# Kernel tuning notes

Measured on AMD Instinct MI355X. Metric: run time of the kernel, lower is better.

Reference implementation:

```python
import jax, jax.numpy as jnp
import numpy as np

B, L, D = 4, 2048, 512
H, DK, DV = 8, 64, 64


def setup_inputs() -> dict:
    key = jax.random.key(0)
    ks = jax.random.split(key, 12)
    s = 0.02
    return {
        "query": jax.random.normal(ks[0], (B, L, D), jnp.float32),
        "key": jax.random.normal(ks[1], (B, L, D), jnp.float32),
        "value": jax.random.normal(ks[2], (B, L, D), jnp.float32),
        "attention_mask": jax.random.normal(ks[3], (1, 1, L, L), jnp.float32),
        "Wq": jax.random.normal(ks[4], (D, H * DK), jnp.float32) * s,
        "bq": jnp.zeros((H * DK,), jnp.float32),
        "Wk": jax.random.normal(ks[5], (D, H * DK), jnp.float32) * s,
        "bk": jnp.zeros((H * DK,), jnp.float32),
        "Wv": jax.random.normal(ks[6], (D, H * DV), jnp.float32) * s,
        "bv": jnp.zeros((H * DV,), jnp.float32),
        "Wo": jax.random.normal(ks[7], (H * DV, D), jnp.float32) * s,
        "bo": jnp.zeros((D,), jnp.float32),
    }


def reference(query, key, value, attention_mask, Wq, bq, Wk, bk, Wv, bv, Wo, bo):
    sz_b, len_q, _ = query.shape
    len_k = key.shape[1]
    # projections -> [B, L, H, d]
    q = (query @ Wq + bq).reshape(sz_b, len_q, H, DK)
    k = (key @ Wk + bk).reshape(sz_b, len_k, H, DK)
    v = (value @ Wv + bv).reshape(sz_b, len_k, H, DV)
    # permute(2,0,1,3): heads first -> [H, B, L, d]
    q = jnp.transpose(q, (2, 0, 1, 3))
    k = jnp.transpose(k, (2, 0, 1, 3))
    v = jnp.transpose(v, (2, 0, 1, 3))
    scale = 1.0 / jnp.sqrt(jnp.asarray(DK, q.dtype))
    scores = jnp.einsum('hbqd,hbkd->hbqk', q, k) * scale + attention_mask
    attn = jax.nn.softmax(scores, axis=-1)
    x = jnp.einsum('hbqk,hbkd->hbqd', attn, v)  # [H, B, Lq, Dv]
    # faithful to torch: transpose(1,2) -> [H, Lq, B, Dv] then view(B, Lq, H*Dv)
    x = jnp.transpose(x, (0, 2, 1, 3)).reshape(sz_b, len_q, H * DV)
    return x @ Wo + bo
```

## Files before the change

kernel.cpp:

```cpp
#include <hip/hip_runtime.h>

#define SEQ    2048
#define DMODEL 512
#define NHEAD  8
#define HDIM   64
#define BATCH  4

#define LOG2E  1.4426950408889634f
#define QSCALE 0.18033688011112042f

typedef float f32x4  __attribute__((ext_vector_type(4)));
typedef float f32x16 __attribute__((ext_vector_type(16)));
typedef _Float16 h16x8 __attribute__((ext_vector_type(8)));
typedef _Float16 h16x2 __attribute__((ext_vector_type(2)));

union U4H { uint4 u; h16x8 h; };
union U1H2 { unsigned int u; h16x2 h; };

static __device__ inline h16x2 pkrtz(float a, float b) {
    return __builtin_bit_cast(h16x2, __builtin_amdgcn_cvt_pkrtz(a, b));
}
static __device__ inline unsigned short f2h(float x) {
    _Float16 h = (_Float16)x;
    return __builtin_bit_cast(unsigned short, h);
}
static __device__ inline void async_cp16(const void* g, void* l) {
    __builtin_amdgcn_global_load_lds(
        (const __attribute__((address_space(1))) unsigned int*)g,
        (__attribute__((address_space(3))) unsigned int*)l,
        16, 0, 0);
}

__global__ __launch_bounds__(256) void transpose_cast_w(
    const float* __restrict__ s0, const float* __restrict__ s1,
    const float* __restrict__ s2, const float* __restrict__ s3,
    unsigned short* __restrict__ d0, unsigned short* __restrict__ d1,
    unsigned short* __restrict__ d2, unsigned short* __restrict__ d3)
{
    const float* S; unsigned short* D;
    switch (blockIdx.z) {
        case 0: S = s0; D = d0; break;
        case 1: S = s1; D = d1; break;
        case 2: S = s2; D = d2; break;
        default: S = s3; D = d3; break;
    }
    __shared__ float T[32][33];
    const int t = threadIdx.x;
    const int r = t >> 3, c = (t & 7) * 4;
    const int k0 = blockIdx.x * 32, n0 = blockIdx.y * 32;
    float4 v = *(const float4*)&S[(size_t)(k0 + r) * DMODEL + n0 + c];
    T[r][c] = v.x; T[r][c + 1] = v.y; T[r][c + 2] = v.z; T[r][c + 3] = v.w;
    __syncthreads();
    ushort4 o;
    o.x = f2h(T[c + 0][r]); o.y = f2h(T[c + 1][r]);
    o.z = f2h(T[c + 2][r]); o.w = f2h(T[c + 3][r]);
    *(ushort4*)&D[(size_t)(n0 + r) * DMODEL + k0 + c] = o;
}

__global__ __launch_bounds__(256) void prep_mask(
    const float* __restrict__ mask, unsigned short* __restrict__ mp)
{
    int i = blockIdx.x * 256 + threadIdx.x;
    int k = (i * 4) & (SEQ - 1);
    int q = (i * 4) >> 11;
    float4 v = ((const float4*)mask)[i];
    int kt = k >> 6, kl = k & 63;
    int mt = kl >> 5, g = (kl >> 3) & 3, hl = (kl >> 2) & 1;
    size_t base = ((size_t)kt * SEQ + q) * 64 + hl * 32 + mt * 16 + g * 4;
    ushort4 o;
    o.x = f2h(__builtin_amdgcn_exp2f(v.x * LOG2E));
    o.y = f2h(__builtin_amdgcn_exp2f(v.y * LOG2E));
    o.z = f2h(__builtin_amdgcn_exp2f(v.z * LOG2E));
    o.w = f2h(__builtin_amdgcn_exp2f(v.w * LOG2E));
    *(ushort4*)&mp[base] = o;
}

__global__ __launch_bounds__(256) void transpose_v(
    const unsigned short* __restrict__ vb, unsigned short* __restrict__ vT)
{
    const int t = threadIdx.x;
    const int key0 = blockIdx.x * 64;
    const int bh = blockIdx.y, b = bh >> 3, h = bh & 7;
    #pragma unroll
    for (int p = 0; p < 2; p++) {
        int cid = p * 256 + t;
        int dv = cid >> 3, kch = cid & 7;
        unsigned short tmp[8];
        #pragma unroll
        for (int j = 0; j < 8; j++)
            tmp[j] = vb[(size_t)(b * SEQ + key0 + kch * 8 + j) * DMODEL + h * HDIM + dv];
        uint4 o;
        o.x = tmp[0] | ((unsigned)tmp[1] << 16);
        o.y = tmp[2] | ((unsigned)tmp[3] << 16);
        o.z = tmp[4] | ((unsigned)tmp[5] << 16);
        o.w = tmp[6] | ((unsigned)tmp[7] << 16);
        *(uint4*)&vT[(size_t)((b * NHEAD + h) * HDIM + dv) * SEQ + key0 + kch * 8] = o;
    }
}

template <int A_FP32, int OUT_F16>
static __device__ inline void gemm_core(
    const void* __restrict__ Ap, const unsigned short* __restrict__ Bt,
    const float* __restrict__ bias, void* __restrict__ Cout, float oscale,
    int bm, int bn)
{
    __shared__ __align__(16) unsigned short As[128 * 32];
    __shared__ __align__(16) unsigned short Bs[128 * 32];

    const int t = threadIdx.x;
    const int lane = t & 63, w = t >> 6;
    const int wm = w >> 1, wn = w & 1;
    const int c = lane & 15, quad = lane >> 4;

    f32x4 acc[4][4] = {};

    for (int k0 = 0; k0 < DMODEL; k0 += 32) {
        if (A_FP32) {
            const float* Af = (const float*)Ap;
            #pragma unroll
            for (int p = 0; p < 4; p++) {
                int cid = p * 256 + t;
                int row = cid >> 3, fc = cid & 7;
                float4 av = *(const float4*)&Af[(size_t)(bm + row) * DMODEL + k0 + fc * 4];
                U1H2 lo, hi;
                lo.h = pkrtz(av.x, av.y);
                hi.h = pkrtz(av.z, av.w);
                uint2 st = make_uint2(lo.u, hi.u);
                *(uint2*)&As[row * 32 + fc * 4] = st;
            }
        } else {
            const unsigned short* Ab = (const unsigned short*)Ap;
            #pragma unroll
            for (int i = 0; i < 2; i++) {
                int row = 32 * w + 16 * i + (lane >> 2);
                const unsigned short* gp = Ab + (size_t)(bm + row) * DMODEL + k0 + (lane & 3) * 8;
                async_cp16(gp, &As[(32 * w + 16 * i) * 32]);
            }
        }
        #pragma unroll
        for (int i = 0; i < 2; i++) {
            int row = 32 * w + 16 * i + (lane >> 2);
            const unsigned short* gp = Bt + (size_t)(bn + row) * DMODEL + k0 + (lane & 3) * 8;
            async_cp16(gp, &Bs[(32 * w + 16 * i) * 32]);
        }
        __syncthreads();

        U4H af[4], bf[4];
        #pragma unroll
        for (int mt = 0; mt < 4; mt++)
            af[mt].u = *(const uint4*)&As[(wm * 64 + mt * 16 + c) * 32 + quad * 8];
        #pragma unroll
        for (int nt = 0; nt < 4; nt++)
            bf[nt].u = *(const uint4*)&Bs[(wn * 64 + nt * 16 + c) * 32 + quad * 8];
        #pragma unroll
        for (int mt = 0; mt < 4; mt++)
            #pragma unroll
            for (int nt = 0; nt < 4; nt++)
                acc[mt][nt] = __builtin_amdgcn_mfma_f32_16x16x32_f16(
                    af[mt].h, bf[nt].h, acc[mt][nt], 0, 0, 0);
        __syncthreads();
    }

    #pragma unroll
    for (int nt = 0; nt < 4; nt++) {
        int ng = bn + wn * 64 + nt * 16 + c;
        float bv = bias[ng];
        #pragma unroll
        for (int mt = 0; mt < 4; mt++) {
            #pragma unroll
            for (int r = 0; r < 4; r++) {
                int mg = bm + wm * 64 + mt * 16 + quad * 4 + r;
                float v = (acc[mt][nt][r] + bv) * oscale;
                if (OUT_F16)
                    ((unsigned short*)Cout)[(size_t)mg * DMODEL + ng] = f2h(v);
                else
                    ((float*)Cout)[(size_t)mg * DMODEL + ng] = v;
            }
        }
    }
}

struct QKVArgs {
    const float *A0, *A1, *A2;
    const unsigned short *W0, *W1, *W2;
    const float *b0, *b1, *b2;
    unsigned short *o0, *o1, *o2;
};

__global__ __launch_bounds__(256) void gemm_qkv(QKVArgs a) {
    const float* A; const unsigned short* W; const float* bias;
    unsigned short* out; float sc;
    switch (blockIdx.z) {
        case 0: A = a.A0; W = a.W0; bias = a.b0; out = a.o0; sc = QSCALE; break;
        case 1: A = a.A1; W = a.W1; bias = a.b1; out = a.o1; sc = 1.0f;  break;
        default: A = a.A2; W = a.W2; bias = a.b2; out = a.o2; sc = 1.0f; break;
    }
    gemm_core<1, 1>(A, W, bias, out, sc, blockIdx.y * 128, blockIdx.x * 128);
}

__global__ __launch_bounds__(256) void gemm_fin(
    const unsigned short* __restrict__ A, const unsigned short* __restrict__ W,
    const float* __restrict__ bias, float* __restrict__ C) {
    gemm_core<0, 0>(A, W, bias, C, 1.0f, blockIdx.y * 128, blockIdx.x * 128);
}

__global__ __launch_bounds__(256, 2) void attn4(
    const unsigned short* __restrict__ qb, const unsigned short* __restrict__ kb,
    const unsigned short* __restrict__ vT, const unsigned short* __restrict__ emp,
    unsigned short* __restrict__ X)
{
    __shared__ __align__(16) unsigned short Ks[8 * 65 * 8];
    __shared__ __align__(16) unsigned short Vs[8 * 65 * 8];

    const int t = threadIdx.x;
    const int lane = t & 63, w = t >> 6;
    const int c32 = lane & 31, hl = lane >> 5;
    const int bh = blockIdx.x, b = bh >> 3, head = bh & 7;
    const int q0 = blockIdx.y * 128;
    const int qg = q0 + w * 32 + c32;

    const unsigned short* qrow = qb + ((size_t)b * SEQ + qg) * DMODEL + head * HDIM;
    U4H Qf[4];
    #pragma unroll
    for (int s = 0; s < 4; s++)
        Qf[s].u = *(const uint4*)&qrow[s * 16 + hl * 8];

    const unsigned short* kgb = kb + (size_t)b * SEQ * DMODEL + head * HDIM;
    const unsigned short* vgb = vT + (size_t)bh * HDIM * SEQ;

    const int r8p = t >> 3;
    const int chp = t & 7;

    uint4 kreg[2], vreg[2];
    #pragma unroll
    for (int p = 0; p < 2; p++) {
        int r8 = p * 32 + r8p;
        kreg[p] = *(const uint4*)&kgb[(size_t)r8 * DMODEL + chp * 8];
        vreg[p] = *(const uint4*)&vgb[(size_t)r8 * SEQ + 0 + chp * 8];
    }

    f32x16 O0 = {}, O1 = {};
    float lsum = 0.f;

    for (int kt = 0; kt < SEQ / 64; kt++) {
        __syncthreads();
        #pragma unroll
        for (int p = 0; p < 2; p++) {
            int r8 = p * 32 + r8p;
            *(uint4*)&Ks[(chp * 65 + r8) * 8] = kreg[p];
            *(uint4*)&Vs[(chp * 65 + r8) * 8] = vreg[p];
        }
        __syncthreads();

        if (kt + 1 < SEQ / 64) {
            int k0n = (kt + 1) * 64;
            #pragma unroll
            for (int p = 0; p < 2; p++) {
                int r8 = p * 32 + r8p;
                kreg[p] = *(const uint4*)&kgb[(size_t)(k0n + r8) * DMODEL + chp * 8];
                vreg[p] = *(const uint4*)&vgb[(size_t)r8 * SEQ + k0n + chp * 8];
            }
        }

        const unsigned short* mrow = emp + ((size_t)kt * SEQ + qg) * 64 + hl * 32;
        U4H e0, e1, e2, e3;
        e0.u = *(const uint4*)&mrow[0];
        e1.u = *(const uint4*)&mrow[8];
        e2.u = *(const uint4*)&mrow[16];
        e3.u = *(const uint4*)&mrow[24];

        f32x16 S0 = {}, S1 = {};
        #pragma unroll
        for (int s = 0; s < 4; s++) {
            int fc = 2 * s + hl;
            U4H ka0, ka1;
            ka0.u = *(const uint4*)&Ks[(fc * 65 + c32) * 8];
            ka1.u = *(const uint4*)&Ks[(fc * 65 + 32 + c32) * 8];
            S0 = __builtin_amdgcn_mfma_f32_32x32x16_f16(ka0.h, Qf[s].h, S0, 0, 0, 0);
            S1 = __builtin_amdgcn_mfma_f32_32x32x16_f16(ka1.h, Qf[s].h, S1, 0, 0, 0);
        }

        unsigned int Pf[4][4];
        #pragma unroll
        for (int mt = 0; mt < 2; mt++) {
            f32x16 S = mt ? S1 : S0;
            h16x8 ea = (mt ? e2 : e0).h;
            h16x8 eb = (mt ? e3 : e1).h;
            unsigned int u[4][2];
            #pragma unroll
            for (int jj = 0; jj < 8; jj++) {
                _Float16 exl = (jj < 4) ? ea[2 * jj]     : eb[2 * jj - 8];
                _Float16 exh = (jj < 4) ? ea[2 * jj + 1] : eb[2 * jj - 7];
                h16x2 ex = {exl, exh};
                h16x2 pk = pkrtz(__builtin_amdgcn_exp2f(S[2 * jj]),
                                 __builtin_amdgcn_exp2f(S[2 * jj + 1]));
                h16x2 pp = pk * ex;
                lsum += (float)pp[0] + (float)pp[1];
                u[jj >> 1][jj & 1] = __builtin_bit_cast(unsigned int, pp);
            }
            unsigned int sA0 = hl ? u[0][0] : u[1][0];
            unsigned int sA1 = hl ? u[0][1] : u[1][1];
            unsigned int sB0 = hl ? u[2][0] : u[3][0];
            unsigned int sB1 = hl ? u[2][1] : u[3][1];
            unsigned int rA0 = (unsigned)__shfl_xor((int)sA0, 32, 64);
            unsigned int rA1 = (unsigned)__shfl_xor((int)sA1, 32, 64);
            unsigned int rB0 = (unsigned)__shfl_xor((int)sB0, 32, 64);
            unsigned int rB1 = (unsigned)__shfl_xor((int)sB1, 32, 64);
            Pf[2 * mt + 0][0] = hl ? rA0 : u[0][0];
            Pf[2 * mt + 0][1] = hl ? rA1 : u[0][1];
            Pf[2 * mt + 0][2] = hl ? u[1][0] : rA0;
            Pf[2 * mt + 0][3] = hl ? u[1][1] : rA1;
            Pf[2 * mt + 1][0] = hl ? rB0 : u[2][0];
            Pf[2 * mt + 1][1] = hl ? rB1 : u[2][1];
            Pf[2 * mt + 1][2] = hl ? u[3][0] : rB0;
            Pf[2 * mt + 1][3] = hl ? u[3][1] : rB1;
        }

        #pragma unroll
        for (int s = 0; s < 4; s++) {
            int kc = 2 * s + hl;
            U4H va0, va1, pu;
            va0.u = *(const uint4*)&Vs[(kc * 65 + c32) * 8];
            va1.u = *(const uint4*)&Vs[(kc * 65 + 32 + c32) * 8];
            pu.u = make_uint4(Pf[s][0], Pf[s][1], Pf[s][2], Pf[s][3]);
            O0 = __builtin_amdgcn_mfma_f32_32x32x16_f16(va0.h, pu.h, O0, 0, 0, 0);
            O1 = __builtin_amdgcn_mfma_f32_32x32x16_f16(va1.h, pu.h, O1, 0, 0, 0);
        }
    }

    lsum += __shfl_xor(lsum, 32, 64);
    float inv = 1.0f / lsum;
    unsigned short* xrow = X + (((size_t)head * SEQ + qg) * BATCH + b) * HDIM;
    #pragma unroll
    for (int mt = 0; mt < 2; mt++) {
        f32x16 Ov = mt ? O1 : O0;
        #pragma unroll
        for (int g = 0; g < 4; g++) {
            U1H2 lo, hi;
            lo.h = pkrtz(Ov[g * 4 + 0] * inv, Ov[g * 4 + 1] * inv);
            hi.h = pkrtz(Ov[g * 4 + 2] * inv, Ov[g * 4 + 3] * inv);
            uint2 st = make_uint2(lo.u, hi.u);
            *(uint2*)&xrow[mt * 32 + 8 * g + 4 * hl] = st;
        }
    }
}

extern "C" void kernel_launch(void* const* d_in, const int* in_sizes, int n_in,
                              void* d_out, int out_size, void* d_ws, size_t ws_size,
                              hipStream_t stream) {
    const float* query = (const float*)d_in[0];
    const float* key_  = (const float*)d_in[1];
    const float* value = (const float*)d_in[2];
    const float* mask  = (const float*)d_in[3];
    const float* Wq = (const float*)d_in[4];
    const float* bq = (const float*)d_in[5];
    const float* Wk = (const float*)d_in[6];
    const float* bk = (const float*)d_in[7];
    const float* Wv = (const float*)d_in[8];
    const float* bv = (const float*)d_in[9];
    const float* Wo = (const float*)d_in[10];
    const float* bo = (const float*)d_in[11];
    float* out = (float*)d_out;

    const size_t NP = (size_t)BATCH * SEQ * DMODEL;
    unsigned short* ws   = (unsigned short*)d_ws;
    unsigned short* qb16 = ws;
    unsigned short* kb16 = qb16 + NP;
    unsigned short* vb16 = kb16 + NP;
    unsigned short* vT16 = vb16 + NP;
    unsigned short* xb16 = vT16 + NP;
    unsigned short* em16 = xb16 + NP;
    unsigned short* WqT  = em16 + (size_t)SEQ * SEQ;
    unsigned short* WkT  = WqT + DMODEL * DMODEL;
    unsigned short* WvT  = WkT + DMODEL * DMODEL;
    unsigned short* WoT  = WvT + DMODEL * DMODEL;

    transpose_cast_w<<<dim3(16, 16, 4), 256, 0, stream>>>(
        Wq, Wk, Wv, Wo, WqT, WkT, WvT, WoT);
    prep_mask<<<dim3(SEQ * SEQ / 4 / 256), 256, 0, stream>>>(mask, em16);

    QKVArgs qa;
    qa.A0 = query; qa.A1 = key_; qa.A2 = value;
    qa.W0 = WqT;   qa.W1 = WkT;  qa.W2 = WvT;
    qa.b0 = bq;    qa.b1 = bk;   qa.b2 = bv;
    qa.o0 = qb16;  qa.o1 = kb16; qa.o2 = vb16;
    gemm_qkv<<<dim3(DMODEL / 128, BATCH * SEQ / 128, 3), 256, 0, stream>>>(qa);

    transpose_v<<<dim3(SEQ / 64, BATCH * NHEAD), 256, 0, stream>>>(vb16, vT16);

    attn4<<<dim3(BATCH * NHEAD, SEQ / 128), 256, 0, stream>>>(
        qb16, kb16, vT16, em16, xb16);

    gemm_fin<<<dim3(DMODEL / 128, BATCH * SEQ / 128), 256, 0, stream>>>(
        xb16, WoT, bo, out);
}
```

Measured before the change: 265.1 us.

## Split attention over keys, async double-buffer K/V, fuse V transpose into GEMM

The attention kernel now splits the key range in two across a grid z-dimension, writes unnormalized partial outputs and row sums, and adds a combine kernel that merges them. K/V tiles are loaded with async global-to-LDS copies into a double-buffered, XOR-swizzled shared layout instead of going through registers. The V projection GEMM writes the transposed layout directly, which removes the separate transpose_v pass, and occupancy is raised to 3 blocks per CU. This adds parallelism and overlap of memory with compute, at the cost of an extra kernel, extra traffic for the partial results, and fp16 rounding of the unnormalized partials.

Result: faster. 253.1 us (-4.5%).

```diff
diff --git a/kernel.cpp b/kernel.cpp
--- a/kernel.cpp
+++ b/kernel.cpp
@@ -5,6 +5,8 @@
 #define NHEAD  8
 #define HDIM   64
 #define BATCH  4
+#define NROWS  65536
+#define KSPLIT 2
 
 #define LOG2E  1.4426950408889634f
 #define QSCALE 0.18033688011112042f
@@ -75,30 +77,7 @@
     *(ushort4*)&mp[base] = o;
 }
 
-__global__ __launch_bounds__(256) void transpose_v(
-    const unsigned short* __restrict__ vb, unsigned short* __restrict__ vT)
-{
-    const int t = threadIdx.x;
-    const int key0 = blockIdx.x * 64;
-    const int bh = blockIdx.y, b = bh >> 3, h = bh & 7;
-    #pragma unroll
-    for (int p = 0; p < 2; p++) {
-        int cid = p * 256 + t;
-        int dv = cid >> 3, kch = cid & 7;
-        unsigned short tmp[8];
-        #pragma unroll
-        for (int j = 0; j < 8; j++)
-            tmp[j] = vb[(size_t)(b * SEQ + key0 + kch * 8 + j) * DMODEL + h * HDIM + dv];
-        uint4 o;
-        o.x = tmp[0] | ((unsigned)tmp[1] << 16);
-        o.y = tmp[2] | ((unsigned)tmp[3] << 16);
-        o.z = tmp[4] | ((unsigned)tmp[5] << 16);
-        o.w = tmp[6] | ((unsigned)tmp[7] << 16);
-        *(uint4*)&vT[(size_t)((b * NHEAD + h) * HDIM + dv) * SEQ + key0 + kch * 8] = o;
-    }
-}
-
-template <int A_FP32, int OUT_F16>
+template <int A_FP32, int EPI>
 static __device__ inline void gemm_core(
     const void* __restrict__ Ap, const unsigned short* __restrict__ Bt,
     const float* __restrict__ bias, void* __restrict__ Cout, float oscale,
@@ -161,6 +140,26 @@
         __syncthreads();
     }
 
+    if (EPI == 2) {
+        #pragma unroll
+        for (int nt = 0; nt < 4; nt++) {
+            int ng = bn + wn * 64 + nt * 16 + c;
+            int h = ng >> 6, dv = ng & 63;
+            float bv = bias[ng];
+            #pragma unroll
+            for (int mt = 0; mt < 4; mt++) {
+                int mg0 = bm + wm * 64 + mt * 16 + quad * 4;
+                int bb = mg0 >> 11, key0 = mg0 & (SEQ - 1);
+                U1H2 lo, hi;
+                lo.h = pkrtz(acc[mt][nt][0] + bv, acc[mt][nt][1] + bv);
+                hi.h = pkrtz(acc[mt][nt][2] + bv, acc[mt][nt][3] + bv);
+                *(uint2*)&((unsigned short*)Cout)[
+                    ((size_t)(bb * NHEAD + h) * HDIM + dv) * SEQ + key0] =
+                    make_uint2(lo.u, hi.u);
+            }
+        }
+        return;
+    }
     #pragma unroll
     for (int nt = 0; nt < 4; nt++) {
         int ng = bn + wn * 64 + nt * 16 + c;
@@ -171,7 +170,7 @@
             for (int r = 0; r < 4; r++) {
                 int mg = bm + wm * 64 + mt * 16 + quad * 4 + r;
                 float v = (acc[mt][nt][r] + bv) * oscale;
-                if (OUT_F16)
+                if (EPI == 1)
                     ((unsigned short*)Cout)[(size_t)mg * DMODEL + ng] = f2h(v);
                 else
                     ((float*)Cout)[(size_t)mg * DMODEL + ng] = v;
@@ -188,14 +187,12 @@
 };
 
 __global__ __launch_bounds__(256) void gemm_qkv(QKVArgs a) {
-    const float* A; const unsigned short* W; const float* bias;
-    unsigned short* out; float sc;
-    switch (blockIdx.z) {
-        case 0: A = a.A0; W = a.W0; bias = a.b0; out = a.o0; sc = QSCALE; break;
-        case 1: A = a.A1; W = a.W1; bias = a.b1; out = a.o1; sc = 1.0f;  break;
-        default: A = a.A2; W = a.W2; bias = a.b2; out = a.o2; sc = 1.0f; break;
-    }
-    gemm_core<1, 1>(A, W, bias, out, sc, blockIdx.y * 128, blockIdx.x * 128);
+    if (blockIdx.z == 2)
+        gemm_core<1, 2>(a.A2, a.W2, a.b2, a.o2, 1.0f, blockIdx.y * 128, blockIdx.x * 128);
+    else if (blockIdx.z == 1)
+        gemm_core<1, 1>(a.A1, a.W1, a.b1, a.o1, 1.0f, blockIdx.y * 128, blockIdx.x * 128);
+    else
+        gemm_core<1, 1>(a.A0, a.W0, a.b0, a.o0, QSCALE, blockIdx.y * 128, blockIdx.x * 128);
 }
 
 __global__ __launch_bounds__(256) void gemm_fin(
@@ -204,19 +201,20 @@
     gemm_core<0, 0>(A, W, bias, C, 1.0f, blockIdx.y * 128, blockIdx.x * 128);
 }
 
-__global__ __launch_bounds__(256, 2) void attn4(
+__global__ __launch_bounds__(256, 3) void attn5(
     const unsigned short* __restrict__ qb, const unsigned short* __restrict__ kb,
     const unsigned short* __restrict__ vT, const unsigned short* __restrict__ emp,
-    unsigned short* __restrict__ X)
+    unsigned short* __restrict__ Xp, float* __restrict__ Lp)
 {
-    __shared__ __align__(16) unsigned short Ks[8 * 65 * 8];
-    __shared__ __align__(16) unsigned short Vs[8 * 65 * 8];
+    __shared__ __align__(16) unsigned short Ks[2][64 * 64];
+    __shared__ __align__(16) unsigned short Vs[2][64 * 64];
 
     const int t = threadIdx.x;
     const int lane = t & 63, w = t >> 6;
     const int c32 = lane & 31, hl = lane >> 5;
     const int bh = blockIdx.x, b = bh >> 3, head = bh & 7;
     const int q0 = blockIdx.y * 128;
+    const int split = blockIdx.z;
     const int qg = q0 + w * 32 + c32;
 
     const unsigned short* qrow = qb + ((size_t)b * SEQ + qg) * DMODEL + head * HDIM;
@@ -225,57 +223,60 @@
     for (int s = 0; s < 4; s++)
         Qf[s].u = *(const uint4*)&qrow[s * 16 + hl * 8];
 
-    const unsigned short* kgb = kb + (size_t)b * SEQ * DMODEL + head * HDIM;
-    const unsigned short* vgb = vT + (size_t)bh * HDIM * SEQ;
-
-    const int r8p = t >> 3;
-    const int chp = t & 7;
-
-    uint4 kreg[2], vreg[2];
-    #pragma unroll
-    for (int p = 0; p < 2; p++) {
-        int r8 = p * 32 + r8p;
-        kreg[p] = *(const uint4*)&kgb[(size_t)r8 * DMODEL + chp * 8];
-        vreg[p] = *(const uint4*)&vgb[(size_t)r8 * SEQ + 0 + chp * 8];
+    const unsigned short* kgb = kb + (size_t)b * SEQ * DMODEL + head * HDIM
+                              + (size_t)split * 1024 * DMODEL;
+    const unsigned short* vgb = vT + (size_t)bh * HDIM * SEQ + split * 1024;
+
+    const int srow = lane >> 3;
+    const int sch  = (lane & 7) ^ srow;
+
+    {
+        #pragma unroll
+        for (int i = 0; i < 2; i++) {
+            int row = w * 16 + i * 8 + srow;
+            async_cp16(&kgb[(size_t)row * DMODEL + sch * 8], &Ks[0][(w * 16 + i * 8) * 64]);
+            async_cp16(&vgb[(size_t)row * SEQ + sch * 8],    &Vs[0][(w * 16 + i * 8) * 64]);
+        }
     }
 
     f32x16 O0 = {}, O1 = {};
     float lsum = 0.f;
 
-    for (int kt = 0; kt < SEQ / 64; kt++) {
+    for (int kt = 0; kt < 1024 / 64; kt++) {
+        const int p = kt & 1;
         __syncthreads();
-        #pragma unroll
-        for (int p = 0; p < 2; p++) {
-            int r8 = p * 32 + r8p;
-            *(uint4*)&Ks[(chp * 65 + r8) * 8] = kreg[p];
-            *(uint4*)&Vs[(chp * 65 + r8) * 8] = vreg[p];
-        }
-        __syncthreads();
-
-        if (kt + 1 < SEQ / 64) {
-            int k0n = (kt + 1) * 64;
-            #pragma unroll
-            for (int p = 0; p < 2; p++) {
-                int r8 = p * 32 + r8p;
-                kreg[p] = *(const uint4*)&kgb[(size_t)(k0n + r8) * DMODEL + chp * 8];
-                vreg[p] = *(const uint4*)&vgb[(size_t)r8 * SEQ + k0n + chp * 8];
-            }
-        }
-
-        const unsigned short* mrow = emp + ((size_t)kt * SEQ + qg) * 64 + hl * 32;
+
+        const int ktg = split * 16 + kt;
+        const unsigned short* mrow = emp + ((size_t)ktg * SEQ + qg) * 64 + hl * 32;
         U4H e0, e1, e2, e3;
         e0.u = *(const uint4*)&mrow[0];
         e1.u = *(const uint4*)&mrow[8];
         e2.u = *(const uint4*)&mrow[16];
         e3.u = *(const uint4*)&mrow[24];
 
+        if (kt + 1 < 1024 / 64) {
+            int k0n = (kt + 1) * 64;
+            #pragma unroll
+            for (int i = 0; i < 2; i++) {
+                int row = w * 16 + i * 8 + srow;
+                async_cp16(&kgb[(size_t)(k0n + row) * DMODEL + sch * 8],
+                           &Ks[p ^ 1][(w * 16 + i * 8) * 64]);
+                async_cp16(&vgb[(size_t)row * SEQ + k0n + sch * 8],
+                           &Vs[p ^ 1][(w * 16 + i * 8) * 64]);
+            }
+        }
+
+        const unsigned short* Kp = Ks[p];
+        const unsigned short* Vp = Vs[p];
+
         f32x16 S0 = {}, S1 = {};
         #pragma unroll
         for (int s = 0; s < 4; s++) {
             int fc = 2 * s + hl;
+            int sl = (fc ^ (c32 & 7)) * 8;
             U4H ka0, ka1;
-            ka0.u = *(const uint4*)&Ks[(fc * 65 + c32) * 8];
-            ka1.u = *(const uint4*)&Ks[(fc * 65 + 32 + c32) * 8];
+            ka0.u = *(const uint4*)&Kp[c32 * 64 + sl];
+            ka1.u = *(const uint4*)&Kp[(32 + c32) * 64 + sl];
             S0 = __builtin_amdgcn_mfma_f32_32x32x16_f16(ka0.h, Qf[s].h, S0, 0, 0, 0);
             S1 = __builtin_amdgcn_mfma_f32_32x32x16_f16(ka1.h, Qf[s].h, S1, 0, 0, 0);
         }
@@ -319,9 +320,10 @@
         #pragma unroll
         for (int s = 0; s < 4; s++) {
             int kc = 2 * s + hl;
+            int sl = (kc ^ (c32 & 7)) * 8;
             U4H va0, va1, pu;
-            va0.u = *(const uint4*)&Vs[(kc * 65 + c32) * 8];
-            va1.u = *(const uint4*)&Vs[(kc * 65 + 32 + c32) * 8];
+            va0.u = *(const uint4*)&Vp[c32 * 64 + sl];
+            va1.u = *(const uint4*)&Vp[(32 + c32) * 64 + sl];
             pu.u = make_uint4(Pf[s][0], Pf[s][1], Pf[s][2], Pf[s][3]);
             O0 = __builtin_amdgcn_mfma_f32_32x32x16_f16(va0.h, pu.h, O0, 0, 0, 0);
             O1 = __builtin_amdgcn_mfma_f32_32x32x16_f16(va1.h, pu.h, O1, 0, 0, 0);
@@ -329,20 +331,42 @@
     }
 
     lsum += __shfl_xor(lsum, 32, 64);
-    float inv = 1.0f / lsum;
-    unsigned short* xrow = X + (((size_t)head * SEQ + qg) * BATCH + b) * HDIM;
+    const size_t j = ((size_t)head * SEQ + qg) * BATCH + b;
+    unsigned short* xr = Xp + ((size_t)split * NROWS + j) * HDIM;
     #pragma unroll
     for (int mt = 0; mt < 2; mt++) {
         f32x16 Ov = mt ? O1 : O0;
         #pragma unroll
         for (int g = 0; g < 4; g++) {
             U1H2 lo, hi;
-            lo.h = pkrtz(Ov[g * 4 + 0] * inv, Ov[g * 4 + 1] * inv);
-            hi.h = pkrtz(Ov[g * 4 + 2] * inv, Ov[g * 4 + 3] * inv);
+            lo.h = pkrtz(Ov[g * 4 + 0], Ov[g * 4 + 1]);
+            hi.h = pkrtz(Ov[g * 4 + 2], Ov[g * 4 + 3]);
             uint2 st = make_uint2(lo.u, hi.u);
-            *(uint2*)&xrow[mt * 32 + 8 * g + 4 * hl] = st;
-        }
-    }
+            *(uint2*)&xr[mt * 32 + 8 * g + 4 * hl] = st;
+        }
+    }
+    if (hl == 0) Lp[split * NROWS + j] = lsum;
+}
+
+__global__ __launch_bounds__(256) void combine_attn(
+    const unsigned short* __restrict__ Xp, const float* __restrict__ Lp,
+    unsigned short* __restrict__ xb)
+{
+    int i = blockIdx.x * 256 + threadIdx.x;
+    int j = i >> 3, dc = (i & 7) * 8;
+    U4H a, b;
+    a.u = *(const uint4*)&Xp[(size_t)j * HDIM + dc];
+    b.u = *(const uint4*)&Xp[((size_t)NROWS + j) * HDIM + dc];
+    float inv = 1.0f / (Lp[j] + Lp[NROWS + j]);
+    U4H o;
+    #pragma unroll
+    for (int p = 0; p < 4; p++) {
+        float s0 = ((float)a.h[2 * p]     + (float)b.h[2 * p])     * inv;
+        float s1 = ((float)a.h[2 * p + 1] + (float)b.h[2 * p + 1]) * inv;
+        h16x2 pk = pkrtz(s0, s1);
+        o.h[2 * p] = pk[0]; o.h[2 * p + 1] = pk[1];
+    }
+    *(uint4*)&xb[(size_t)j * HDIM + dc] = o.u;
 }
 
 extern "C" void kernel_launch(void* const* d_in, const int* in_sizes, int n_in,
@@ -366,14 +390,15 @@
     unsigned short* ws   = (unsigned short*)d_ws;
     unsigned short* qb16 = ws;
     unsigned short* kb16 = qb16 + NP;
-    unsigned short* vb16 = kb16 + NP;
-    unsigned short* vT16 = vb16 + NP;
+    unsigned short* vT16 = kb16 + NP;
     unsigned short* xb16 = vT16 + NP;
     unsigned short* em16 = xb16 + NP;
-    unsigned short* WqT  = em16 + (size_t)SEQ * SEQ;
+    unsigned short* Xp16 = em16 + (size_t)SEQ * SEQ;
+    unsigned short* WqT  = Xp16 + (size_t)KSPLIT * NROWS * HDIM;
     unsigned short* WkT  = WqT + DMODEL * DMODEL;
     unsigned short* WvT  = WkT + DMODEL * DMODEL;
     unsigned short* WoT  = WvT + DMODEL * DMODEL;
+    float* Lp = (float*)(WoT + DMODEL * DMODEL);
 
     transpose_cast_w<<<dim3(16, 16, 4), 256, 0, stream>>>(
         Wq, Wk, Wv, Wo, WqT, WkT, WvT, WoT);
@@ -383,13 +408,13 @@
     qa.A0 = query; qa.A1 = key_; qa.A2 = value;
     qa.W0 = WqT;   qa.W1 = WkT;  qa.W2 = WvT;
     qa.b0 = bq;    qa.b1 = bk;   qa.b2 = bv;
-    qa.o0 = qb16;  qa.o1 = kb16; qa.o2 = vb16;
+    qa.o0 = qb16;  qa.o1 = kb16; qa.o2 = vT16;
     gemm_qkv<<<dim3(DMODEL / 128, BATCH * SEQ / 128, 3), 256, 0, stream>>>(qa);
 
-    transpose_v<<<dim3(SEQ / 64, BATCH * NHEAD), 256, 0, stream>>>(vb16, vT16);
-
-    attn4<<<dim3(BATCH * NHEAD, SEQ / 128), 256, 0, stream>>>(
-        qb16, kb16, vT16, em16, xb16);
+    attn5<<<dim3(BATCH * NHEAD, SEQ / 128, KSPLIT), 256, 0, stream>>>(
+        qb16, kb16, vT16, em16, Xp16, Lp);
+
+    combine_attn<<<dim3(NROWS * 8 / 256), 256, 0, stream>>>(Xp16, Lp, xb16);
 
     gemm_fin<<<dim3(DMODEL / 128, BATCH * SEQ / 128), 256, 0, stream>>>(
         xb16, WoT, bo, out);
```
